# Optimization experiments

Measured on AMD Instinct MI355X. Metric: run time of the kernel, lower is better.

The kernel has to match this reference:

```python
import jax, jax.numpy as jnp
import numpy as np

N, M, D, DV = 8192, 8192, 64, 64

def setup_inputs() -> dict:
    key = jax.random.key(0)
    kq, kk, kv = jax.random.split(key, 3)
    Q = jax.random.normal(kq, (N, D), dtype=jnp.float32)
    K = jax.random.normal(kk, (M, D), dtype=jnp.float32)
    V = jax.random.normal(kv, (M, DV), dtype=jnp.float32)
    return {"Q": Q, "K": K, "V": V}

def reference(Q, K, V):
    d = K.shape[-1]
    scores = jnp.einsum('nd,md->nm', Q, K) / jnp.sqrt(jnp.float32(d))  # [N, M]
    attn = jax.nn.softmax(scores, axis=-1)
    return attn @ V  # [N, DV]
```

## Files before the change

kernel.cpp:

```cpp
#include <hip/hip_runtime.h>


#define NQ 8192
#define NK 8192

typedef float f32x4 __attribute__((ext_vector_type(4)));
typedef short short8 __attribute__((ext_vector_type(8)));
union U4 { uint4 u; short8 s; };

#define MFMA16 __builtin_amdgcn_mfma_f32_16x16x32_bf16

__device__ __forceinline__ unsigned pk2(float a, float b) {
    unsigned ua = __builtin_bit_cast(unsigned, a);
    unsigned ub = __builtin_bit_cast(unsigned, b);
    ua = (ua + 0x7FFFu + ((ua >> 16) & 1u)) >> 16;
    ub = (ub + 0x7FFFu + ((ub >> 16) & 1u)) & 0xFFFF0000u;
    return ua | ub;
}

__device__ __forceinline__ unsigned pkt(float a, float b) {
    return __builtin_amdgcn_perm(__builtin_bit_cast(unsigned, b),
                                 __builtin_bit_cast(unsigned, a), 0x07060302u);
}

__global__ __launch_bounds__(256)
void prepass(const float* __restrict__ Kg, const float* __restrict__ Vg,
             uint4* __restrict__ Kb4, uint4* __restrict__ Vt4) {
    __shared__ float ld[64 * 33];
    const int t = threadIdx.x, b = blockIdx.x;

    if (b < 256) {
        const int f = t >> 6, l = t & 63;
        const int i16 = l & 15, g = l >> 4;
        const int row = b * 32 + (f >> 1) * 16 + i16;
        const int dg = g + (f & 1) * 4;
        const float* gp = Kg + (size_t)row * 64 + dg * 8;
        float4 f0 = *(const float4*)gp;
        float4 f1 = *(const float4*)(gp + 4);
        uint4 o = make_uint4(pk2(f0.x, f0.y), pk2(f0.z, f0.w),
                             pk2(f1.x, f1.y), pk2(f1.z, f1.w));
        Kb4[(size_t)(b * 4 + f) * 64 + l] = o;
    } else {
        const int c = b - 256;
        {
            const int key = t >> 3, dg = t & 7;
            const float* gp = Vg + (size_t)(c * 32 + key) * 64 + dg * 8;
            float4 f0 = *(const float4*)gp;
            float4 f1 = *(const float4*)(gp + 4);
            ld[(dg * 8 + 0) * 33 + key] = f0.x;
            ld[(dg * 8 + 1) * 33 + key] = f0.y;
            ld[(dg * 8 + 2) * 33 + key] = f0.z;
            ld[(dg * 8 + 3) * 33 + key] = f0.w;
            ld[(dg * 8 + 4) * 33 + key] = f1.x;
            ld[(dg * 8 + 5) * 33 + key] = f1.y;
            ld[(dg * 8 + 6) * 33 + key] = f1.z;
            ld[(dg * 8 + 7) * 33 + key] = f1.w;
        }
        __syncthreads();
        {
            const int dim = t >> 2, kq = t & 3;
            const int dt = dim >> 4, i16 = dim & 15;
            float v[8];
            #pragma unroll
            for (int j = 0; j < 8; ++j) v[j] = ld[dim * 33 + kq * 8 + j];
            uint4 o = make_uint4(pk2(v[0], v[1]), pk2(v[2], v[3]),
                                 pk2(v[4], v[5]), pk2(v[6], v[7]));
            Vt4[(size_t)(c * 4 + dt) * 64 + kq * 16 + i16] = o;
        }
    }
}

__global__ __launch_bounds__(512, 1)
void attn_main(const float* __restrict__ Qg,
               const uint4* __restrict__ Kb4,
               const uint4* __restrict__ Vt4,
               float* __restrict__ Opart,
               float* __restrict__ Lpart) {
    __shared__ float sF[4 * 4160];

    const int t = threadIdx.x, w = t >> 6, lane = t & 63;
    const int q = lane >> 4, i16 = lane & 15;
    const int bid = blockIdx.x;
    const int kh = bid & 1;
    const int rg = bid >> 1;
    const int qb0 = rg * 64;
    const int phase = rg & 15;

    uint4 kfA[4], vfA[4], kfB[4], vfB[4];

#define CBASE(TT) (((kh << 7) + ((((TT) + phase) & 15) * 8 + w)) * 4)

#define LOAD_K(KD, TT)                                                               \
    do {                                                                             \
        const int cb = CBASE(TT);                                                    \
        _Pragma("unroll")                                                            \
        for (int f = 0; f < 4; ++f)                                                  \
            (KD)[f] = Kb4[(size_t)(cb + f) * 64 + lane];                             \
    } while (0)

#define LOAD_V(VD, TT)                                                               \
    do {                                                                             \
        const int cb = CBASE(TT);                                                    \
        _Pragma("unroll")                                                            \
        for (int dt = 0; dt < 4; ++dt)                                               \
            (VD)[dt] = Vt4[(size_t)(cb + dt) * 64 + lane];                           \
    } while (0)

    LOAD_K(kfA, 0); LOAD_V(vfA, 0);
    LOAD_K(kfB, 1); LOAD_V(vfB, 1);

    const float SCL = 0.18033688011112042f;
    short8 aq[4][2];
    #pragma unroll
    for (int rt = 0; rt < 4; ++rt) {
        const float* qp = Qg + (size_t)(qb0 + rt * 16 + i16) * 64 + q * 8;
        float4 f0 = *(const float4*)(qp);
        float4 f1 = *(const float4*)(qp + 4);
        U4 u;
        u.u = make_uint4(pk2(f0.x * SCL, f0.y * SCL), pk2(f0.z * SCL, f0.w * SCL),
                         pk2(f1.x * SCL, f1.y * SCL), pk2(f1.z * SCL, f1.w * SCL));
        aq[rt][0] = u.s;
        f0 = *(const float4*)(qp + 32);
        f1 = *(const float4*)(qp + 36);
        u.u = make_uint4(pk2(f0.x * SCL, f0.y * SCL), pk2(f0.z * SCL, f0.w * SCL),
                         pk2(f1.x * SCL, f1.y * SCL), pk2(f1.z * SCL, f1.w * SCL));
        aq[rt][1] = u.s;
    }

    f32x4 acc[4][4];
    float lsum[4];
    #pragma unroll
    for (int rt = 0; rt < 4; ++rt) {
        #pragma unroll
        for (int dt = 0; dt < 4; ++dt) { acc[rt][dt][0]=0.f; acc[rt][dt][1]=0.f; acc[rt][dt][2]=0.f; acc[rt][dt][3]=0.f; }
        lsum[rt] = 0.f;
    }

#define TILE(KD, VD)                                                                 \
    do {                                                                             \
        _Pragma("unroll")                                                            \
        for (int rt = 0; rt < 4; ++rt) {                                             \
            f32x4 s0, s1;                                                            \
            s0[0]=-16.f; s0[1]=-16.f; s0[2]=-16.f; s0[3]=-16.f;                      \
            s1[0]=-16.f; s1[1]=-16.f; s1[2]=-16.f; s1[3]=-16.f;                      \
            U4 k0, k1, k2, k3;                                                       \
            k0.u = (KD)[0]; k1.u = (KD)[1]; k2.u = (KD)[2]; k3.u = (KD)[3];          \
            s0 = MFMA16(k0.s, aq[rt][0], s0, 0, 0, 0);                               \
            s0 = MFMA16(k1.s, aq[rt][1], s0, 0, 0, 0);                               \
            s1 = MFMA16(k2.s, aq[rt][0], s1, 0, 0, 0);                               \
            s1 = MFMA16(k3.s, aq[rt][1], s1, 0, 0, 0);                               \
            float p00 = __builtin_amdgcn_exp2f(s0[0]);                               \
            float p01 = __builtin_amdgcn_exp2f(s0[1]);                               \
            float p02 = __builtin_amdgcn_exp2f(s0[2]);                               \
            float p03 = __builtin_amdgcn_exp2f(s0[3]);                               \
            float p10 = __builtin_amdgcn_exp2f(s1[0]);                               \
            float p11 = __builtin_amdgcn_exp2f(s1[1]);                               \
            float p12 = __builtin_amdgcn_exp2f(s1[2]);                               \
            float p13 = __builtin_amdgcn_exp2f(s1[3]);                               \
            lsum[rt] += ((p00 + p01) + (p02 + p03)) + ((p10 + p11) + (p12 + p13));   \
            unsigned w0 = pkt(p00, p01), w1 = pkt(p02, p03);                         \
            unsigned w2 = pkt(p10, p11), w3 = pkt(p12, p13);                         \
            asm("v_permlane32_swap_b32 %0, %1" : "+v"(w0), "+v"(w2));                \
            asm("v_permlane16_swap_b32 %0, %1" : "+v"(w0), "+v"(w2));                \
            asm("v_permlane32_swap_b32 %0, %1" : "+v"(w1), "+v"(w3));                \
            asm("v_permlane16_swap_b32 %0, %1" : "+v"(w1), "+v"(w3));                \
            U4 ap; ap.u = make_uint4(w0, w1, w2, w3);                                \
            _Pragma("unroll")                                                        \
            for (int dt = 0; dt < 4; ++dt) {                                         \
                U4 bv; bv.u = (VD)[dt];                                              \
                acc[rt][dt] = MFMA16(ap.s, bv.s, acc[rt][dt], 0, 0, 0);              \
            }                                                                        \
        }                                                                            \
    } while (0)

    #pragma unroll 1
    for (int tt = 0; tt < 14; tt += 2) {
        TILE(kfA, vfA);
        LOAD_K(kfA, tt + 2); LOAD_V(vfA, tt + 2);
        TILE(kfB, vfB);
        LOAD_K(kfB, tt + 3); LOAD_V(vfB, tt + 3);
        __builtin_amdgcn_sched_barrier(0);
    }
    TILE(kfA, vfA);
    TILE(kfB, vfB);

    #pragma unroll
    for (int rt = 0; rt < 4; ++rt) {
        float v = lsum[rt];
        v += __shfl_xor(v, 16);
        v += __shfl_xor(v, 32);
        lsum[rt] = v;
    }

    __syncthreads();
    for (int step = 4; step >= 1; step >>= 1) {
        if (w >= step && w < 2 * step) {
            float* base = sF + (w - step) * 4160;
            #pragma unroll
            for (int rt = 0; rt < 4; ++rt) {
                #pragma unroll
                for (int dt = 0; dt < 4; ++dt)
                    #pragma unroll
                    for (int r = 0; r < 4; ++r)
                        base[(rt * 16 + 4 * q + r) * 64 + dt * 16 + i16] = acc[rt][dt][r];
                if (q == 0) base[4096 + rt * 16 + i16] = lsum[rt];
            }
        }
        __syncthreads();
        if (w < step) {
            const float* base = sF + w * 4160;
            #pragma unroll
            for (int rt = 0; rt < 4; ++rt) {
                #pragma unroll
                for (int dt = 0; dt < 4; ++dt)
                    #pragma unroll
                    for (int r = 0; r < 4; ++r)
                        acc[rt][dt][r] += base[(rt * 16 + 4 * q + r) * 64 + dt * 16 + i16];
                lsum[rt] += base[4096 + rt * 16 + i16];
            }
        }
        __syncthreads();
    }

    if (w == 0) {
        #pragma unroll
        for (int rt = 0; rt < 4; ++rt) {
            #pragma unroll
            for (int dt = 0; dt < 4; ++dt)
                #pragma unroll
                for (int r = 0; r < 4; ++r) {
                    const int row = qb0 + rt * 16 + 4 * q + r;
                    Opart[((size_t)kh * 8192 + row) * 64 + dt * 16 + i16] = acc[rt][dt][r];
                }
            if (q == 0)
                Lpart[kh * 8192 + qb0 + rt * 16 + i16] = lsum[rt];
        }
    }
}

__global__ __launch_bounds__(256)
void merge(const float* __restrict__ Opart, const float* __restrict__ Lpart,
           float* __restrict__ Og) {
    const int idx = blockIdx.x * 256 + threadIdx.x;
    const int row = idx >> 4, seg = idx & 15;
    const float4 a = *(const float4*)(Opart + (size_t)row * 64 + seg * 4);
    const float4 b = *(const float4*)(Opart + ((size_t)8192 + row) * 64 + seg * 4);
    const float inv = 1.0f / (Lpart[row] + Lpart[8192 + row]);
    float4 o;
    o.x = (a.x + b.x) * inv;
    o.y = (a.y + b.y) * inv;
    o.z = (a.z + b.z) * inv;
    o.w = (a.w + b.w) * inv;
    *(float4*)(Og + (size_t)row * 64 + seg * 4) = o;
}

extern "C" void kernel_launch(void* const* d_in, const int* in_sizes, int n_in,
                              void* d_out, int out_size, void* d_ws, size_t ws_size,
                              hipStream_t stream) {
    const float* Q = (const float*)d_in[0];
    const float* K = (const float*)d_in[1];
    const float* V = (const float*)d_in[2];
    float* O = (float*)d_out;
    char* ws = (char*)d_ws;
    uint4* Kb4   = (uint4*)ws;
    uint4* Vt4   = (uint4*)(ws + (1 << 20));
    float* Opart = (float*)(ws + (2 << 20));
    float* Lpart = (float*)(ws + (6 << 20));
    hipLaunchKernelGGL(prepass, dim3(512), dim3(256), 0, stream, K, V, Kb4, Vt4);
    hipLaunchKernelGGL(attn_main, dim3(256), dim3(512), 0, stream, Q, Kb4, Vt4, Opart, Lpart);
    hipLaunchKernelGGL(merge, dim3(512), dim3(256), 0, stream, Opart, Lpart, O);
}
```

Before: 86.81 us.

## Software-pipeline QK/exp of next tile with PV MFMAs of previous tile

```diff
diff --git a/kernel.cpp b/kernel.cpp
--- a/kernel.cpp
+++ b/kernel.cpp
@@ -87,6 +87,7 @@
     const int phase = rg & 15;
 
     uint4 kfA[4], vfA[4], kfB[4], vfB[4];
+    U4 apA[4], apB[4];
 
 #define CBASE(TT) (((kh << 7) + ((((TT) + phase) & 15) * 8 + w)) * 4)
 
@@ -136,7 +137,7 @@
         lsum[rt] = 0.f;
     }
 
-#define TILE(KD, VD)                                                                 \
+#define QKEXP(KD, AP)                                                                \
     do {                                                                             \
         _Pragma("unroll")                                                            \
         for (int rt = 0; rt < 4; ++rt) {                                             \
@@ -164,25 +165,44 @@
             asm("v_permlane16_swap_b32 %0, %1" : "+v"(w0), "+v"(w2));                \
             asm("v_permlane32_swap_b32 %0, %1" : "+v"(w1), "+v"(w3));                \
             asm("v_permlane16_swap_b32 %0, %1" : "+v"(w1), "+v"(w3));                \
-            U4 ap; ap.u = make_uint4(w0, w1, w2, w3);                                \
+            (AP)[rt].u = make_uint4(w0, w1, w2, w3);                                 \
+        }                                                                            \
+    } while (0)
+
+#define PVS(AP, VD)                                                                  \
+    do {                                                                             \
+        _Pragma("unroll")                                                            \
+        for (int dt = 0; dt < 4; ++dt) {                                             \
+            U4 bv; bv.u = (VD)[dt];                                                  \
             _Pragma("unroll")                                                        \
-            for (int dt = 0; dt < 4; ++dt) {                                         \
-                U4 bv; bv.u = (VD)[dt];                                              \
-                acc[rt][dt] = MFMA16(ap.s, bv.s, acc[rt][dt], 0, 0, 0);              \
-            }                                                                        \
+            for (int rt = 0; rt < 4; ++rt)                                           \
+                acc[rt][dt] = MFMA16((AP)[rt].s, bv.s, acc[rt][dt], 0, 0, 0);        \
         }                                                                            \
     } while (0)
 
+    QKEXP(kfA, apA);
+    LOAD_K(kfA, 2);
     #pragma unroll 1
-    for (int tt = 0; tt < 14; tt += 2) {
-        TILE(kfA, vfA);
-        LOAD_K(kfA, tt + 2); LOAD_V(vfA, tt + 2);
-        TILE(kfB, vfB);
-        LOAD_K(kfB, tt + 3); LOAD_V(vfB, tt + 3);
-        __builtin_amdgcn_sched_barrier(0);
-    }
-    TILE(kfA, vfA);
-    TILE(kfB, vfB);
+    for (int tt = 0; tt < 12; tt += 2) {
+        QKEXP(kfB, apB);
+        PVS(apA, vfA);
+        LOAD_K(kfB, tt + 3);
+        LOAD_V(vfA, tt + 2);
+        QKEXP(kfA, apA);
+        PVS(apB, vfB);
+        LOAD_K(kfA, tt + 4);
+        LOAD_V(vfB, tt + 3);
+    }
+    QKEXP(kfB, apB);
+    PVS(apA, vfA);
+    LOAD_K(kfB, 15);
+    LOAD_V(vfA, 14);
+    QKEXP(kfA, apA);
+    PVS(apB, vfB);
+    LOAD_V(vfB, 15);
+    QKEXP(kfB, apB);
+    PVS(apA, vfA);
+    PVS(apB, vfB);
 
     #pragma unroll
     for (int rt = 0; rt < 4; ++rt) {
```

New measurement: 85.97 us (median of 3 runs). About the same (-1.0%).

## Share K/V tiles via LDS double buffer across waves with 8-way key split

Applied to the files above, without the earlier changes.

```diff
diff --git a/kernel.cpp b/kernel.cpp
--- a/kernel.cpp
+++ b/kernel.cpp
@@ -70,171 +70,124 @@
     }
 }
 
-__global__ __launch_bounds__(512, 1)
+__global__ __launch_bounds__(512, 4)
 void attn_main(const float* __restrict__ Qg,
                const uint4* __restrict__ Kb4,
                const uint4* __restrict__ Vt4,
                float* __restrict__ Opart,
                float* __restrict__ Lpart) {
-    __shared__ float sF[4 * 4160];
-
-    const int t = threadIdx.x, w = t >> 6, lane = t & 63;
+    __shared__ uint4 sbuf[2][512];
+
+    const int tix = threadIdx.x, w = tix >> 6, lane = tix & 63;
     const int q = lane >> 4, i16 = lane & 15;
     const int bid = blockIdx.x;
-    const int kh = bid & 1;
-    const int rg = bid >> 1;
-    const int qb0 = rg * 64;
-    const int phase = rg & 15;
-
-    uint4 kfA[4], vfA[4], kfB[4], vfB[4];
-
-#define CBASE(TT) (((kh << 7) + ((((TT) + phase) & 15) * 8 + w)) * 4)
-
-#define LOAD_K(KD, TT)                                                               \
-    do {                                                                             \
-        const int cb = CBASE(TT);                                                    \
-        _Pragma("unroll")                                                            \
-        for (int f = 0; f < 4; ++f)                                                  \
-            (KD)[f] = Kb4[(size_t)(cb + f) * 64 + lane];                             \
-    } while (0)
-
-#define LOAD_V(VD, TT)                                                               \
-    do {                                                                             \
-        const int cb = CBASE(TT);                                                    \
-        _Pragma("unroll")                                                            \
-        for (int dt = 0; dt < 4; ++dt)                                               \
-            (VD)[dt] = Vt4[(size_t)(cb + dt) * 64 + lane];                           \
-    } while (0)
-
-    LOAD_K(kfA, 0); LOAD_V(vfA, 0);
-    LOAD_K(kfB, 1); LOAD_V(vfB, 1);
+    const int kq = bid & 7;
+    const int rg = bid >> 3;
+    const int myrow0 = rg * 128 + w * 16;
+
+#define CHUNK(S) (kq * 32 + (((S) + rg) & 31))
+
+    const uint4* __restrict__ sp = (tix < 256) ? Kb4 : Vt4;
+    const int toff = tix & 255;
+
+    uint4 stN = sp[(size_t)CHUNK(0) * 256 + toff];
+    sbuf[0][tix] = stN;
+    stN = sp[(size_t)CHUNK(1) * 256 + toff];
 
     const float SCL = 0.18033688011112042f;
-    short8 aq[4][2];
-    #pragma unroll
-    for (int rt = 0; rt < 4; ++rt) {
-        const float* qp = Qg + (size_t)(qb0 + rt * 16 + i16) * 64 + q * 8;
+    short8 aq0, aq1;
+    {
+        const float* qp = Qg + (size_t)(myrow0 + i16) * 64 + q * 8;
         float4 f0 = *(const float4*)(qp);
         float4 f1 = *(const float4*)(qp + 4);
         U4 u;
         u.u = make_uint4(pk2(f0.x * SCL, f0.y * SCL), pk2(f0.z * SCL, f0.w * SCL),
                          pk2(f1.x * SCL, f1.y * SCL), pk2(f1.z * SCL, f1.w * SCL));
-        aq[rt][0] = u.s;
+        aq0 = u.s;
         f0 = *(const float4*)(qp + 32);
         f1 = *(const float4*)(qp + 36);
         u.u = make_uint4(pk2(f0.x * SCL, f0.y * SCL), pk2(f0.z * SCL, f0.w * SCL),
                          pk2(f1.x * SCL, f1.y * SCL), pk2(f1.z * SCL, f1.w * SCL));
-        aq[rt][1] = u.s;
-    }
-
-    f32x4 acc[4][4];
-    float lsum[4];
+        aq1 = u.s;
+    }
+
+    f32x4 acc[4];
+    float lsum = 0.f;
     #pragma unroll
-    for (int rt = 0; rt < 4; ++rt) {
-        #pragma unroll
-        for (int dt = 0; dt < 4; ++dt) { acc[rt][dt][0]=0.f; acc[rt][dt][1]=0.f; acc[rt][dt][2]=0.f; acc[rt][dt][3]=0.f; }
-        lsum[rt] = 0.f;
-    }
-
-#define TILE(KD, VD)                                                                 \
+    for (int dt = 0; dt < 4; ++dt) { acc[dt][0]=0.f; acc[dt][1]=0.f; acc[dt][2]=0.f; acc[dt][3]=0.f; }
+
+    __syncthreads();
+
+#define TILE_COMPUTE(CUR)                                                            \
     do {                                                                             \
-        _Pragma("unroll")                                                            \
-        for (int rt = 0; rt < 4; ++rt) {                                             \
-            f32x4 s0, s1;                                                            \
-            s0[0]=-16.f; s0[1]=-16.f; s0[2]=-16.f; s0[3]=-16.f;                      \
-            s1[0]=-16.f; s1[1]=-16.f; s1[2]=-16.f; s1[3]=-16.f;                      \
-            U4 k0, k1, k2, k3;                                                       \
-            k0.u = (KD)[0]; k1.u = (KD)[1]; k2.u = (KD)[2]; k3.u = (KD)[3];          \
-            s0 = MFMA16(k0.s, aq[rt][0], s0, 0, 0, 0);                               \
-            s0 = MFMA16(k1.s, aq[rt][1], s0, 0, 0, 0);                               \
-            s1 = MFMA16(k2.s, aq[rt][0], s1, 0, 0, 0);                               \
-            s1 = MFMA16(k3.s, aq[rt][1], s1, 0, 0, 0);                               \
-            float p00 = __builtin_amdgcn_exp2f(s0[0]);                               \
-            float p01 = __builtin_amdgcn_exp2f(s0[1]);                               \
-            float p02 = __builtin_amdgcn_exp2f(s0[2]);                               \
-            float p03 = __builtin_amdgcn_exp2f(s0[3]);                               \
-            float p10 = __builtin_amdgcn_exp2f(s1[0]);                               \
-            float p11 = __builtin_amdgcn_exp2f(s1[1]);                               \
-            float p12 = __builtin_amdgcn_exp2f(s1[2]);                               \
-            float p13 = __builtin_amdgcn_exp2f(s1[3]);                               \
-            lsum[rt] += ((p00 + p01) + (p02 + p03)) + ((p10 + p11) + (p12 + p13));   \
-            unsigned w0 = pkt(p00, p01), w1 = pkt(p02, p03);                         \
-            unsigned w2 = pkt(p10, p11), w3 = pkt(p12, p13);                         \
-            asm("v_permlane32_swap_b32 %0, %1" : "+v"(w0), "+v"(w2));                \
-            asm("v_permlane16_swap_b32 %0, %1" : "+v"(w0), "+v"(w2));                \
-            asm("v_permlane32_swap_b32 %0, %1" : "+v"(w1), "+v"(w3));                \
-            asm("v_permlane16_swap_b32 %0, %1" : "+v"(w1), "+v"(w3));                \
-            U4 ap; ap.u = make_uint4(w0, w1, w2, w3);                                \
-            _Pragma("unroll")                                                        \
-            for (int dt = 0; dt < 4; ++dt) {                                         \
-                U4 bv; bv.u = (VD)[dt];                                              \
-                acc[rt][dt] = MFMA16(ap.s, bv.s, acc[rt][dt], 0, 0, 0);              \
-            }                                                                        \
-        }                                                                            \
+        uint4 kf0 = sbuf[CUR][0 * 64 + lane];                                        \
+        uint4 kf1 = sbuf[CUR][1 * 64 + lane];                                        \
+        uint4 kf2 = sbuf[CUR][2 * 64 + lane];                                        \
+        uint4 kf3 = sbuf[CUR][3 * 64 + lane];                                        \
+        f32x4 s0, s1;                                                                \
+        s0[0]=-16.f; s0[1]=-16.f; s0[2]=-16.f; s0[3]=-16.f;                          \
+        s1[0]=-16.f; s1[1]=-16.f; s1[2]=-16.f; s1[3]=-16.f;                          \
+        U4 k0, k1, k2, k3;                                                           \
+        k0.u = kf0; k1.u = kf1; k2.u = kf2; k3.u = kf3;                              \
+        s0 = MFMA16(k0.s, aq0, s0, 0, 0, 0);                                         \
+        s0 = MFMA16(k1.s, aq1, s0, 0, 0, 0);                                         \
+        s1 = MFMA16(k2.s, aq0, s1, 0, 0, 0);                                         \
+        s1 = MFMA16(k3.s, aq1, s1, 0, 0, 0);                                         \
+        float p00 = __builtin_amdgcn_exp2f(s0[0]);                                   \
+        float p01 = __builtin_amdgcn_exp2f(s0[1]);                                   \
+        float p02 = __builtin_amdgcn_exp2f(s0[2]);                                   \
+        float p03 = __builtin_amdgcn_exp2f(s0[3]);                                   \
+        float p10 = __builtin_amdgcn_exp2f(s1[0]);                                   \
+        float p11 = __builtin_amdgcn_exp2f(s1[1]);                                   \
+        float p12 = __builtin_amdgcn_exp2f(s1[2]);                                   \
+        float p13 = __builtin_amdgcn_exp2f(s1[3]);                                   \
+        lsum += ((p00 + p01) + (p02 + p03)) + ((p10 + p11) + (p12 + p13));           \
+        unsigned w0 = pkt(p00, p01), w1 = pkt(p02, p03);                             \
+        unsigned w2 = pkt(p10, p11), w3 = pkt(p12, p13);                             \
+        asm("v_permlane32_swap_b32 %0, %1" : "+v"(w0), "+v"(w2));                    \
+        asm("v_permlane16_swap_b32 %0, %1" : "+v"(w0), "+v"(w2));                    \
+        asm("v_permlane32_swap_b32 %0, %1" : "+v"(w1), "+v"(w3));                    \
+        asm("v_permlane16_swap_b32 %0, %1" : "+v"(w1), "+v"(w3));                    \
+        U4 ap; ap.u = make_uint4(w0, w1, w2, w3);                                    \
+        uint4 vf0 = sbuf[CUR][256 + 0 * 64 + lane];                                  \
+        uint4 vf1 = sbuf[CUR][256 + 1 * 64 + lane];                                  \
+        uint4 vf2 = sbuf[CUR][256 + 2 * 64 + lane];                                  \
+        uint4 vf3 = sbuf[CUR][256 + 3 * 64 + lane];                                  \
+        U4 b0, b1, b2, b3;                                                           \
+        b0.u = vf0; b1.u = vf1; b2.u = vf2; b3.u = vf3;                              \
+        acc[0] = MFMA16(ap.s, b0.s, acc[0], 0, 0, 0);                                \
+        acc[1] = MFMA16(ap.s, b1.s, acc[1], 0, 0, 0);                                \
+        acc[2] = MFMA16(ap.s, b2.s, acc[2], 0, 0, 0);                                \
+        acc[3] = MFMA16(ap.s, b3.s, acc[3], 0, 0, 0);                                \
     } while (0)
 
+    int cur = 0;
     #pragma unroll 1
-    for (int tt = 0; tt < 14; tt += 2) {
-        TILE(kfA, vfA);
-        LOAD_K(kfA, tt + 2); LOAD_V(vfA, tt + 2);
-        TILE(kfB, vfB);
-        LOAD_K(kfB, tt + 3); LOAD_V(vfB, tt + 3);
-        __builtin_amdgcn_sched_barrier(0);
-    }
-    TILE(kfA, vfA);
-    TILE(kfB, vfB);
-
-    #pragma unroll
-    for (int rt = 0; rt < 4; ++rt) {
-        float v = lsum[rt];
+    for (int s = 0; s < 31; ++s) {
+        sbuf[cur ^ 1][tix] = stN;
+        stN = sp[(size_t)CHUNK((s + 2) & 31) * 256 + toff];
+        TILE_COMPUTE(cur);
+        __syncthreads();
+        cur ^= 1;
+    }
+    TILE_COMPUTE(cur);
+
+    {
+        float v = lsum;
         v += __shfl_xor(v, 16);
         v += __shfl_xor(v, 32);
-        lsum[rt] = v;
-    }
-
-    __syncthreads();
-    for (int step = 4; step >= 1; step >>= 1) {
-        if (w >= step && w < 2 * step) {
-            float* base = sF + (w - step) * 4160;
+        lsum = v;
+    }
+
+    {
+        const int orow0 = myrow0 + 4 * q;
+        #pragma unroll
+        for (int dt = 0; dt < 4; ++dt)
             #pragma unroll
-            for (int rt = 0; rt < 4; ++rt) {
-                #pragma unroll
-                for (int dt = 0; dt < 4; ++dt)
-                    #pragma unroll
-                    for (int r = 0; r < 4; ++r)
-                        base[(rt * 16 + 4 * q + r) * 64 + dt * 16 + i16] = acc[rt][dt][r];
-                if (q == 0) base[4096 + rt * 16 + i16] = lsum[rt];
-            }
-        }
-        __syncthreads();
-        if (w < step) {
-            const float* base = sF + w * 4160;
-            #pragma unroll
-            for (int rt = 0; rt < 4; ++rt) {
-                #pragma unroll
-                for (int dt = 0; dt < 4; ++dt)
-                    #pragma unroll
-                    for (int r = 0; r < 4; ++r)
-                        acc[rt][dt][r] += base[(rt * 16 + 4 * q + r) * 64 + dt * 16 + i16];
-                lsum[rt] += base[4096 + rt * 16 + i16];
-            }
-        }
-        __syncthreads();
-    }
-
-    if (w == 0) {
-        #pragma unroll
-        for (int rt = 0; rt < 4; ++rt) {
-            #pragma unroll
-            for (int dt = 0; dt < 4; ++dt)
-                #pragma unroll
-                for (int r = 0; r < 4; ++r) {
-                    const int row = qb0 + rt * 16 + 4 * q + r;
-                    Opart[((size_t)kh * 8192 + row) * 64 + dt * 16 + i16] = acc[rt][dt][r];
-                }
-            if (q == 0)
-                Lpart[kh * 8192 + qb0 + rt * 16 + i16] = lsum[rt];
-        }
+            for (int r = 0; r < 4; ++r)
+                Opart[((size_t)kq * 8192 + orow0 + r) * 64 + dt * 16 + i16] = acc[dt][r];
+        if (q == 0)
+            Lpart[kq * 8192 + myrow0 + i16] = lsum;
     }
 }
 
@@ -243,14 +196,16 @@
            float* __restrict__ Og) {
     const int idx = blockIdx.x * 256 + threadIdx.x;
     const int row = idx >> 4, seg = idx & 15;
-    const float4 a = *(const float4*)(Opart + (size_t)row * 64 + seg * 4);
-    const float4 b = *(const float4*)(Opart + ((size_t)8192 + row) * 64 + seg * 4);
-    const float inv = 1.0f / (Lpart[row] + Lpart[8192 + row]);
-    float4 o;
-    o.x = (a.x + b.x) * inv;
-    o.y = (a.y + b.y) * inv;
-    o.z = (a.z + b.z) * inv;
-    o.w = (a.w + b.w) * inv;
+    float4 o; o.x = 0.f; o.y = 0.f; o.z = 0.f; o.w = 0.f;
+    float l = 0.f;
+    #pragma unroll
+    for (int p = 0; p < 8; ++p) {
+        const float4 a = *(const float4*)(Opart + ((size_t)p * 8192 + row) * 64 + seg * 4);
+        o.x += a.x; o.y += a.y; o.z += a.z; o.w += a.w;
+        l += Lpart[p * 8192 + row];
+    }
+    const float inv = 1.0f / l;
+    o.x *= inv; o.y *= inv; o.z *= inv; o.w *= inv;
     *(float4*)(Og + (size_t)row * 64 + seg * 4) = o;
 }
 
@@ -265,8 +220,8 @@
     uint4* Kb4   = (uint4*)ws;
     uint4* Vt4   = (uint4*)(ws + (1 << 20));
     float* Opart = (float*)(ws + (2 << 20));
-    float* Lpart = (float*)(ws + (6 << 20));
+    float* Lpart = (float*)(ws + (18 << 20));
     hipLaunchKernelGGL(prepass, dim3(512), dim3(256), 0, stream, K, V, Kb4, Vt4);
-    hipLaunchKernelGGL(attn_main, dim3(256), dim3(512), 0, stream, Q, Kb4, Vt4, Opart, Lpart);
+    hipLaunchKernelGGL(attn_main, dim3(512), dim3(512), 0, stream, Q, Kb4, Vt4, Opart, Lpart);
     hipLaunchKernelGGL(merge, dim3(512), dim3(256), 0, stream, Opart, Lpart, O);
 }
```

Result: slower. 90.68 us (+4.5%).
